# Optimization experiments

Measured on AMD Instinct MI355X. Metric: run time of the kernel, lower is better.

## Reference

```python
import jax, jax.numpy as jnp
import numpy as np

B, S, D, H = 8, 384, 1024, 16
MAX_SEQ_LEN = 512  # XLRelativePositionalEncoding default -> table rows = 2*512-1 = 1023


def setup_inputs() -> dict:
    key = jax.random.key(0)
    ks = jax.random.split(key, 6)
    x = jax.random.normal(ks[0], (B, S, D), jnp.float32)
    qkv_w = jax.random.normal(ks[1], (D, 3 * D), jnp.float32) / np.float32(np.sqrt(D))
    qkv_b = jnp.zeros((3 * D,), jnp.float32)
    out_w = jax.random.normal(ks[2], (D, D), jnp.float32) / np.float32(np.sqrt(D))
    out_b = jnp.zeros((D,), jnp.float32)
    rpe_table = jax.random.normal(ks[3], (2 * MAX_SEQ_LEN - 1, D), jnp.float32) * 0.02
    return {"x": x, "qkv_w": qkv_w, "qkv_b": qkv_b, "out_w": out_w, "out_b": out_b, "rpe_table": rpe_table}


def reference(x, qkv_w, qkv_b, out_w, out_b, rpe_table):
    b, s, d = x.shape
    h = H
    hd = d // h  # head dim (d_k)

    # XL relative positional embeddings: rpe[i, j] = j - i + s, looked up in table
    pe = jnp.arange(s)
    rpe_idx = (pe[None, :] - pe[:, None]) + s  # (s, s) int indices
    rpem = rpe_table[rpe_idx]                   # (s, s, d)
    rpem = rpem.reshape(h, s, s, hd)            # same raw reshape as source

    # QKV projection
    qkv = x @ qkv_w + qkv_b                     # (b, s, 3d)
    qkv = qkv.reshape(b, s, h, 3 * hd).transpose(0, 2, 1, 3)  # (b, h, s, 3*hd)
    q, k, v = jnp.split(qkv, 3, axis=-1)        # each (b, h, s, hd)

    # scaled dot-product with XL relative bias
    scale = jnp.float32(1.0) / jnp.sqrt(jnp.float32(hd))
    logits = jnp.einsum('bhsd,bhkd->bhsk', q, k) * scale
    logits = logits + jnp.einsum('bhsd,hskd->bhsk', q, rpem)
    attention = jax.nn.softmax(logits, axis=-1)  # (b, h, s, s)
    values = jnp.einsum('bhsk,bhkd->bhsd', attention, v)

    values = values.transpose(0, 2, 1, 3).reshape(b, s, d)
    out = values @ out_w + out_b                 # (b, s, d)
    return out, attention
```

## Files before the change

### kernel.cpp

```cpp
#include <hip/hip_runtime.h>

#define S_ 384
#define D_ 1024
#define H_ 16
#define HD_ 64

typedef short bf16x8 __attribute__((ext_vector_type(8)));
typedef float f32x4 __attribute__((ext_vector_type(4)));

#define LDS_AS3(p) ((__attribute__((address_space(3))) unsigned int*)(p))
#define GLB_AS1(p) ((const __attribute__((address_space(1))) unsigned int*)(p))

__device__ __forceinline__ unsigned short f32_to_bf16(float f) {
  unsigned u = __float_as_uint(f);
  u += 0x7FFFu + ((u >> 16) & 1u);
  return (unsigned short)(u >> 16);
}
__device__ __forceinline__ float bf16_to_f32(unsigned short h) {
  return __uint_as_float(((unsigned)h) << 16);
}

__global__ void cast_kernel(const float* __restrict__ src,
                            unsigned short* __restrict__ dst, int n4) {
  int i = blockIdx.x * blockDim.x + threadIdx.x;
  if (i >= n4) return;
  float4 v = ((const float4*)src)[i];
  ushort4 o;
  o.x = f32_to_bf16(v.x); o.y = f32_to_bf16(v.y);
  o.z = f32_to_bf16(v.z); o.w = f32_to_bf16(v.w);
  ((ushort4*)dst)[i] = o;
}

__global__ void transpose_cast_kernel(const float* __restrict__ W,
                                      unsigned short* __restrict__ Wt,
                                      int K, int N) {
  __shared__ float tile[32][33];
  int n0 = blockIdx.x * 32, k0 = blockIdx.y * 32;
  int tx = threadIdx.x, ty = threadIdx.y;
#pragma unroll
  for (int yy = 0; yy < 32; yy += 8)
    tile[ty + yy][tx] = W[(size_t)(k0 + ty + yy) * N + n0 + tx];
  __syncthreads();
#pragma unroll
  for (int yy = 0; yy < 32; yy += 8)
    Wt[(size_t)(n0 + ty + yy) * K + k0 + tx] = f32_to_bf16(tile[tx][ty + yy]);
}

template <int MODE>
__global__ __launch_bounds__(256) void gemm_bt_kernel(
    const unsigned short* __restrict__ A, const unsigned short* __restrict__ Bt,
    const float* __restrict__ bias, unsigned short* __restrict__ Qb,
    unsigned short* __restrict__ Kb, unsigned short* __restrict__ Vt,
    float* __restrict__ Cout) {
  const int K = 1024;
  __shared__ __align__(16) unsigned short As[128 * 32];
  __shared__ __align__(16) unsigned short Bs[128 * 32];
  const int tid = threadIdx.x;
  const int m0 = blockIdx.x * 128, n0 = blockIdx.y * 128;
  const int wid = tid >> 6, lane = tid & 63;
  const int wr = wid >> 1, wc = wid & 1;
  const int l15 = lane & 15, lg = lane >> 4;

  const int r0 = tid >> 2, kk0 = (tid & 3) * 8;
  const int r1 = (256 + tid) >> 2, kk1 = (tid & 3) * 8;

  f32x4 acc[4][4];
#pragma unroll
  for (int m = 0; m < 4; ++m)
#pragma unroll
    for (int n = 0; n < 4; ++n) acc[m][n] = (f32x4){0.f, 0.f, 0.f, 0.f};

  for (int k0 = 0; k0 < K; k0 += 32) {
    __syncthreads();
    {
      char* asb = (char*)As + (wid << 10);
      char* bsb = (char*)Bs + (wid << 10);
      __builtin_amdgcn_global_load_lds(
          GLB_AS1(&A[(size_t)(m0 + r0) * K + k0 + kk0]), LDS_AS3(asb), 16, 0, 0);
      __builtin_amdgcn_global_load_lds(
          GLB_AS1(&Bt[(size_t)(n0 + r0) * K + k0 + kk0]), LDS_AS3(bsb), 16, 0, 0);
      __builtin_amdgcn_global_load_lds(
          GLB_AS1(&A[(size_t)(m0 + r1) * K + k0 + kk1]), LDS_AS3(asb + 4096), 16, 0, 0);
      __builtin_amdgcn_global_load_lds(
          GLB_AS1(&Bt[(size_t)(n0 + r1) * K + k0 + kk1]), LDS_AS3(bsb + 4096), 16, 0, 0);
    }
    __syncthreads();
    bf16x8 af[4], bf[4];
#pragma unroll
    for (int m = 0; m < 4; ++m)
      af[m] = *(bf16x8*)&As[(wr * 64 + m * 16 + l15) * 32 + lg * 8];
#pragma unroll
    for (int n = 0; n < 4; ++n)
      bf[n] = *(bf16x8*)&Bs[(wc * 64 + n * 16 + l15) * 32 + lg * 8];
#pragma unroll
    for (int m = 0; m < 4; ++m)
#pragma unroll
      for (int n = 0; n < 4; ++n)
        acc[m][n] =
            __builtin_amdgcn_mfma_f32_16x16x32_bf16(af[m], bf[n], acc[m][n], 0, 0, 0);
  }

#pragma unroll
  for (int m = 0; m < 4; ++m) {
#pragma unroll
    for (int n = 0; n < 4; ++n) {
#pragma unroll
      for (int r = 0; r < 4; ++r) {
        int R = m0 + wr * 64 + m * 16 + lg * 4 + r;
        int c = n0 + wc * 64 + n * 16 + l15;
        float val = acc[m][n][r] + bias[c];
        if (MODE == 0) {
          int b = R / S_, s = R % S_;
          int hh = c / 192, rr = c % 192;
          int sel = rr >> 6, dd = rr & 63;
          unsigned short bv = f32_to_bf16(val);
          if (sel == 0) {
            Qb[((size_t)(b * H_ + hh) * S_ + s) * HD_ + dd] = bv;
          } else if (sel == 1) {
            Kb[((size_t)(b * H_ + hh) * S_ + s) * HD_ + dd] = bv;
          } else {
            Vt[((size_t)(b * H_ + hh) * HD_ + dd) * S_ + s] = bv;
          }
        } else {
          Cout[(size_t)R * D_ + c] = val;
        }
      }
    }
  }
}

__global__ __launch_bounds__(512) void bias_kernel(
    const unsigned short* __restrict__ Qb, const unsigned short* __restrict__ Tb,
    unsigned short* __restrict__ biasout) {
  __shared__ __align__(16) unsigned short tb[8][8][136];
  const int hh = blockIdx.x;
  const int itile = blockIdx.y;
  const int jz = blockIdx.z;
  const int tid = threadIdx.x;
  const int wid = tid >> 6, lane = tid & 63;
  const int l15 = lane & 15, lg = lane >> 4;
  const int C = 384 - 24 * hh - itile;
  const int i0 = itile * 16;

#pragma unroll
  for (int t = 0; t < 2; ++t) {
    const int il = wid * 2 + t;
    const int i = i0 + il;
    const int b8 = l15 & 7;
    const size_t qaddr = ((size_t)(b8 * H_ + hh) * S_ + i) * HD_ + lg * 8;
    bf16x8 a0 = *(const bf16x8*)&Qb[qaddr];
    bf16x8 a1 = *(const bf16x8*)&Qb[qaddr + 32];
    const int rbase = il * 24 + C;
#pragma unroll
    for (int jrel = 0; jrel < 8; ++jrel) {
      const int jH = jz * 8 + jrel;
      const unsigned short* trow = Tb + (size_t)(rbase + jH) * D_;
      bf16x8 b0 = *(const bf16x8*)&trow[l15 * 64 + lg * 8];
      bf16x8 b1 = *(const bf16x8*)&trow[l15 * 64 + 32 + lg * 8];
      f32x4 d = {0.f, 0.f, 0.f, 0.f};
      d = __builtin_amdgcn_mfma_f32_16x16x32_bf16(a0, b0, d, 0, 0, 0);
      d = __builtin_amdgcn_mfma_f32_16x16x32_bf16(a1, b1, d, 0, 0, 0);
      if (lg < 2) {
#pragma unroll
        for (int rr = 0; rr < 4; ++rr)
          tb[wid][lg * 4 + rr][jrel * 16 + l15] = f32_to_bf16(d[rr]);
      }
    }
    __syncthreads();
    {
      const int b = lane >> 3;
      const int jseg = (lane & 7) * 16;
      uint4 v0 = *(const uint4*)&tb[wid][b][jseg];
      uint4 v1 = *(const uint4*)&tb[wid][b][jseg + 8];
      unsigned short* dst =
          &biasout[(((size_t)(b * H_ + hh)) * S_ + i) * S_ + jz * 128 + jseg];
      *(uint4*)dst = v0;
      *(uint4*)&dst[8] = v1;
    }
    __syncthreads();
  }
}

__global__ __launch_bounds__(256) void attn2_kernel(
    const unsigned short* __restrict__ Qb, const unsigned short* __restrict__ Kb,
    const unsigned short* __restrict__ Vt, const unsigned short* __restrict__ Bias,
    float* __restrict__ attn_out, unsigned short* __restrict__ Vals) {
  __shared__ float lgs[16][392];
  __shared__ __align__(16) unsigned short pb[16][392];
  const int bh = blockIdx.x;
  const int itile = blockIdx.y;
  const int i0 = itile * 16;
  const size_t base = (size_t)bh * (S_ * HD_);
  const int tid = threadIdx.x, wid = tid >> 6, lane = tid & 63;
  const int l15 = lane & 15, lg = lane >> 4;

  {
    const unsigned short* bsrc = Bias + ((size_t)bh * S_ + i0) * S_;
#pragma unroll
    for (int it = 0; it < 3; ++it) {
      int e = it * 256 + tid;
      int row = e / 48, col = (e % 48) * 8;
      *(uint4*)&pb[row][col] = *(const uint4*)&bsrc[(size_t)row * S_ + col];
    }
  }

  const size_t qaddr = base + (size_t)(i0 + l15) * HD_ + lg * 8;
  bf16x8 qa0 = *(const bf16x8*)&Qb[qaddr];
  bf16x8 qa1 = *(const bf16x8*)&Qb[qaddr + 32];
  __syncthreads();

#pragma unroll
  for (int t = 0; t < 6; ++t) {
    const int jH = wid * 6 + t;
    const int j0 = jH * 16;
    const size_t kaddr = base + (size_t)(j0 + l15) * HD_ + lg * 8;
    bf16x8 kb0 = *(const bf16x8*)&Kb[kaddr];
    bf16x8 kb1 = *(const bf16x8*)&Kb[kaddr + 32];
    f32x4 d = {0.f, 0.f, 0.f, 0.f};
    d = __builtin_amdgcn_mfma_f32_16x16x32_bf16(qa0, kb0, d, 0, 0, 0);
    d = __builtin_amdgcn_mfma_f32_16x16x32_bf16(qa1, kb1, d, 0, 0, 0);
#pragma unroll
    for (int rr = 0; rr < 4; ++rr) {
      const int il = lg * 4 + rr;
      lgs[il][j0 + l15] = d[rr] * 0.125f + bf16_to_f32(pb[il][j0 + l15]);
    }
  }
  __syncthreads();

  {
    const int row = tid >> 4, l16 = tid & 15;
    float m = -1e30f;
    for (int j = l16; j < S_; j += 16) m = fmaxf(m, lgs[row][j]);
#pragma unroll
    for (int o = 8; o; o >>= 1) m = fmaxf(m, __shfl_xor(m, o, 16));
    float s = 0.f;
    for (int j = l16; j < S_; j += 16) {
      float e = __expf(lgs[row][j] - m);
      lgs[row][j] = e;
      s += e;
    }
#pragma unroll
    for (int o = 8; o; o >>= 1) s += __shfl_xor(s, o, 16);
    const float inv = 1.0f / s;
    float* ao = attn_out + ((size_t)bh * S_ + i0 + row) * S_;
    for (int j = l16; j < S_; j += 16) {
      float p = lgs[row][j] * inv;
      ao[j] = p;
      pb[row][j] = f32_to_bf16(p);
    }
  }
  __syncthreads();

  {
    const int d0 = wid * 16;
    f32x4 acc = {0.f, 0.f, 0.f, 0.f};
#pragma unroll 4
    for (int kc = 0; kc < 12; ++kc) {
      bf16x8 pa = *(const bf16x8*)&pb[l15][kc * 32 + lg * 8];
      bf16x8 vb = *(const bf16x8*)&Vt[base + (size_t)(d0 + l15) * S_ + kc * 32 + lg * 8];
      acc = __builtin_amdgcn_mfma_f32_16x16x32_bf16(pa, vb, acc, 0, 0, 0);
    }
    const int b = bh >> 4, hh = bh & 15;
#pragma unroll
    for (int rr = 0; rr < 4; ++rr) {
      const int il = lg * 4 + rr;
      Vals[((size_t)(b * S_ + i0 + il)) * D_ + hh * HD_ + d0 + l15] =
          f32_to_bf16(acc[rr]);
    }
  }
}

extern "C" void kernel_launch(void* const* d_in, const int* in_sizes, int n_in,
                              void* d_out, int out_size, void* d_ws,
                              size_t ws_size, hipStream_t stream) {
  (void)in_sizes; (void)n_in; (void)out_size; (void)ws_size;
  const float* x     = (const float*)d_in[0];
  const float* qkv_w = (const float*)d_in[1];
  const float* qkv_b = (const float*)d_in[2];
  const float* out_w = (const float*)d_in[3];
  const float* out_b = (const float*)d_in[4];
  const float* rpe   = (const float*)d_in[5];

  float* out  = (float*)d_out;
  float* attn = out + 3145728;

  unsigned short* ws  = (unsigned short*)d_ws;
  unsigned short* xb  = ws;
  unsigned short* Wt  = xb + 3145728;
  unsigned short* Wot = Wt + 3145728;
  unsigned short* Tb  = Wot + 1048576;
  unsigned short* Qb  = Tb + 1047552;
  unsigned short* Kb  = Qb + 3145728;
  unsigned short* Vt  = Kb + 3145728;
  unsigned short* Vals = Vt + 3145728;
  unsigned short* Bias = Vals + 3145728;

  cast_kernel<<<3072, 256, 0, stream>>>(x, xb, 786432);
  cast_kernel<<<1023, 256, 0, stream>>>(rpe, Tb, 261888);
  transpose_cast_kernel<<<dim3(96, 32), dim3(32, 8), 0, stream>>>(qkv_w, Wt, 1024, 3072);
  transpose_cast_kernel<<<dim3(32, 32), dim3(32, 8), 0, stream>>>(out_w, Wot, 1024, 1024);

  gemm_bt_kernel<0><<<dim3(24, 24), 256, 0, stream>>>(xb, Wt, qkv_b, Qb, Kb, Vt, nullptr);

  bias_kernel<<<dim3(16, 24, 3), 512, 0, stream>>>(Qb, Tb, Bias);

  attn2_kernel<<<dim3(128, 24), 256, 0, stream>>>(Qb, Kb, Vt, Bias, attn, Vals);

  gemm_bt_kernel<1><<<dim3(24, 8), 256, 0, stream>>>(Vals, Wot, out_b, nullptr, nullptr, nullptr, out);
}
```

Measured before the change: 264.6 us.

## Fuse prep cast kernels and double attention row tile to reuse K/V

Merges the two cast and two transpose-cast launches into one prep kernel, removing three launches. The attention kernel now handles 32 query rows per block instead of 16, so each K and V fragment loaded from global memory feeds two MFMA row tiles. The bias is preloaded into the fp32 logits buffer, which is then reused as bf16 storage for the probabilities. This halves the attention grid and raises LDS use per block, which may lower occupancy.

```diff
diff --git a/kernel.cpp b/kernel.cpp
--- a/kernel.cpp
+++ b/kernel.cpp
@@ -20,30 +20,39 @@
   return __uint_as_float(((unsigned)h) << 16);
 }
 
-__global__ void cast_kernel(const float* __restrict__ src,
-                            unsigned short* __restrict__ dst, int n4) {
-  int i = blockIdx.x * blockDim.x + threadIdx.x;
-  if (i >= n4) return;
-  float4 v = ((const float4*)src)[i];
-  ushort4 o;
-  o.x = f32_to_bf16(v.x); o.y = f32_to_bf16(v.y);
-  o.z = f32_to_bf16(v.z); o.w = f32_to_bf16(v.w);
-  ((ushort4*)dst)[i] = o;
-}
-
-__global__ void transpose_cast_kernel(const float* __restrict__ W,
-                                      unsigned short* __restrict__ Wt,
-                                      int K, int N) {
+__global__ __launch_bounds__(256) void prep_kernel(
+    const float* __restrict__ x, const float* __restrict__ rpe,
+    const float* __restrict__ qkv_w, const float* __restrict__ out_w,
+    unsigned short* __restrict__ xb, unsigned short* __restrict__ Tb,
+    unsigned short* __restrict__ Wt, unsigned short* __restrict__ Wot) {
   __shared__ float tile[32][33];
-  int n0 = blockIdx.x * 32, k0 = blockIdx.y * 32;
-  int tx = threadIdx.x, ty = threadIdx.y;
-#pragma unroll
-  for (int yy = 0; yy < 32; yy += 8)
-    tile[ty + yy][tx] = W[(size_t)(k0 + ty + yy) * N + n0 + tx];
-  __syncthreads();
-#pragma unroll
-  for (int yy = 0; yy < 32; yy += 8)
-    Wt[(size_t)(n0 + ty + yy) * K + k0 + tx] = f32_to_bf16(tile[tx][ty + yy]);
+  const int bx = blockIdx.x;
+  const int tid = threadIdx.x;
+  if (bx < 4095) {
+    const float* src = (bx < 3072) ? x : rpe;
+    unsigned short* dst = (bx < 3072) ? xb : Tb;
+    int i = (bx < 3072 ? bx : bx - 3072) * 256 + tid;
+    float4 v = ((const float4*)src)[i];
+    ushort4 o;
+    o.x = f32_to_bf16(v.x); o.y = f32_to_bf16(v.y);
+    o.z = f32_to_bf16(v.z); o.w = f32_to_bf16(v.w);
+    ((ushort4*)dst)[i] = o;
+  } else {
+    const float* W; unsigned short* WT; int N, bb;
+    if (bx < 7167) { W = qkv_w; WT = Wt; N = 3072; bb = bx - 4095; }
+    else           { W = out_w; WT = Wot; N = 1024; bb = bx - 7167; }
+    const int K = 1024;
+    const int nblk = N / 32;
+    const int n0 = (bb % nblk) * 32, k0 = (bb / nblk) * 32;
+    const int tx = tid & 31, ty = tid >> 5;
+#pragma unroll
+    for (int yy = 0; yy < 32; yy += 8)
+      tile[ty + yy][tx] = W[(size_t)(k0 + ty + yy) * N + n0 + tx];
+    __syncthreads();
+#pragma unroll
+    for (int yy = 0; yy < 32; yy += 8)
+      WT[(size_t)(n0 + ty + yy) * K + k0 + tx] = f32_to_bf16(tile[tx][ty + yy]);
+  }
 }
 
 template <int MODE>
@@ -181,54 +190,69 @@
   }
 }
 
-__global__ __launch_bounds__(256) void attn2_kernel(
+__global__ __launch_bounds__(256) void attn3_kernel(
     const unsigned short* __restrict__ Qb, const unsigned short* __restrict__ Kb,
     const unsigned short* __restrict__ Vt, const unsigned short* __restrict__ Bias,
     float* __restrict__ attn_out, unsigned short* __restrict__ Vals) {
-  __shared__ float lgs[16][392];
-  __shared__ __align__(16) unsigned short pb[16][392];
+  __shared__ float lgs[32][408];
   const int bh = blockIdx.x;
-  const int itile = blockIdx.y;
-  const int i0 = itile * 16;
+  const int it32 = blockIdx.y;
+  const int i0 = it32 * 32;
   const size_t base = (size_t)bh * (S_ * HD_);
   const int tid = threadIdx.x, wid = tid >> 6, lane = tid & 63;
   const int l15 = lane & 15, lg = lane >> 4;
 
+  bf16x8 qa[2][2];
+#pragma unroll
+  for (int mt = 0; mt < 2; ++mt) {
+    const size_t qaddr = base + (size_t)(i0 + mt * 16 + l15) * HD_ + lg * 8;
+    qa[mt][0] = *(const bf16x8*)&Qb[qaddr];
+    qa[mt][1] = *(const bf16x8*)&Qb[qaddr + 32];
+  }
+
   {
     const unsigned short* bsrc = Bias + ((size_t)bh * S_ + i0) * S_;
 #pragma unroll
-    for (int it = 0; it < 3; ++it) {
+    for (int it = 0; it < 6; ++it) {
       int e = it * 256 + tid;
-      int row = e / 48, col = (e % 48) * 8;
-      *(uint4*)&pb[row][col] = *(const uint4*)&bsrc[(size_t)row * S_ + col];
-    }
-  }
-
-  const size_t qaddr = base + (size_t)(i0 + l15) * HD_ + lg * 8;
-  bf16x8 qa0 = *(const bf16x8*)&Qb[qaddr];
-  bf16x8 qa1 = *(const bf16x8*)&Qb[qaddr + 32];
+      int row = e / 48, c8 = (e % 48) * 8;
+      ushort4 v0 = *(const ushort4*)&bsrc[(size_t)row * S_ + c8];
+      ushort4 v1 = *(const ushort4*)&bsrc[(size_t)row * S_ + c8 + 4];
+      float4 f0 = {bf16_to_f32(v0.x), bf16_to_f32(v0.y),
+                   bf16_to_f32(v0.z), bf16_to_f32(v0.w)};
+      float4 f1 = {bf16_to_f32(v1.x), bf16_to_f32(v1.y),
+                   bf16_to_f32(v1.z), bf16_to_f32(v1.w)};
+      *(float4*)&lgs[row][c8] = f0;
+      *(float4*)&lgs[row][c8 + 4] = f1;
+    }
+  }
   __syncthreads();
 
 #pragma unroll
   for (int t = 0; t < 6; ++t) {
-    const int jH = wid * 6 + t;
-    const int j0 = jH * 16;
+    const int j0 = (wid * 6 + t) * 16;
     const size_t kaddr = base + (size_t)(j0 + l15) * HD_ + lg * 8;
     bf16x8 kb0 = *(const bf16x8*)&Kb[kaddr];
     bf16x8 kb1 = *(const bf16x8*)&Kb[kaddr + 32];
-    f32x4 d = {0.f, 0.f, 0.f, 0.f};
-    d = __builtin_amdgcn_mfma_f32_16x16x32_bf16(qa0, kb0, d, 0, 0, 0);
-    d = __builtin_amdgcn_mfma_f32_16x16x32_bf16(qa1, kb1, d, 0, 0, 0);
-#pragma unroll
-    for (int rr = 0; rr < 4; ++rr) {
-      const int il = lg * 4 + rr;
-      lgs[il][j0 + l15] = d[rr] * 0.125f + bf16_to_f32(pb[il][j0 + l15]);
+#pragma unroll
+    for (int mt = 0; mt < 2; ++mt) {
+      f32x4 d = {0.f, 0.f, 0.f, 0.f};
+      d = __builtin_amdgcn_mfma_f32_16x16x32_bf16(qa[mt][0], kb0, d, 0, 0, 0);
+      d = __builtin_amdgcn_mfma_f32_16x16x32_bf16(qa[mt][1], kb1, d, 0, 0, 0);
+#pragma unroll
+      for (int rr = 0; rr < 4; ++rr) {
+        const int il = mt * 16 + lg * 4 + rr;
+        lgs[il][j0 + l15] = fmaf(d[rr], 0.125f, lgs[il][j0 + l15]);
+      }
     }
   }
   __syncthreads();
 
-  {
-    const int row = tid >> 4, l16 = tid & 15;
+  unsigned short* us = (unsigned short*)&lgs[0][0];
+#pragma unroll
+  for (int p = 0; p < 2; ++p) {
+    const int row = p * 16 + (tid >> 4);
+    const int l16 = tid & 15;
     float m = -1e30f;
     for (int j = l16; j < S_; j += 16) m = fmaxf(m, lgs[row][j]);
 #pragma unroll
@@ -244,29 +268,36 @@
     const float inv = 1.0f / s;
     float* ao = attn_out + ((size_t)bh * S_ + i0 + row) * S_;
     for (int j = l16; j < S_; j += 16) {
-      float p = lgs[row][j] * inv;
-      ao[j] = p;
-      pb[row][j] = f32_to_bf16(p);
+      float pv = lgs[row][j] * inv;
+      ao[j] = pv;
+      us[row * 816 + j] = f32_to_bf16(pv);
     }
   }
   __syncthreads();
 
   {
     const int d0 = wid * 16;
-    f32x4 acc = {0.f, 0.f, 0.f, 0.f};
-#pragma unroll 4
+    f32x4 acc[2] = {{0.f, 0.f, 0.f, 0.f}, {0.f, 0.f, 0.f, 0.f}};
+#pragma unroll
     for (int kc = 0; kc < 12; ++kc) {
-      bf16x8 pa = *(const bf16x8*)&pb[l15][kc * 32 + lg * 8];
-      bf16x8 vb = *(const bf16x8*)&Vt[base + (size_t)(d0 + l15) * S_ + kc * 32 + lg * 8];
-      acc = __builtin_amdgcn_mfma_f32_16x16x32_bf16(pa, vb, acc, 0, 0, 0);
+      bf16x8 vb =
+          *(const bf16x8*)&Vt[base + (size_t)(d0 + l15) * S_ + kc * 32 + lg * 8];
+#pragma unroll
+      for (int mt = 0; mt < 2; ++mt) {
+        bf16x8 pa =
+            *(const bf16x8*)&us[(size_t)(mt * 16 + l15) * 816 + kc * 32 + lg * 8];
+        acc[mt] = __builtin_amdgcn_mfma_f32_16x16x32_bf16(pa, vb, acc[mt], 0, 0, 0);
+      }
     }
     const int b = bh >> 4, hh = bh & 15;
 #pragma unroll
-    for (int rr = 0; rr < 4; ++rr) {
-      const int il = lg * 4 + rr;
-      Vals[((size_t)(b * S_ + i0 + il)) * D_ + hh * HD_ + d0 + l15] =
-          f32_to_bf16(acc[rr]);
-    }
+    for (int mt = 0; mt < 2; ++mt)
+#pragma unroll
+      for (int rr = 0; rr < 4; ++rr) {
+        const int il = mt * 16 + lg * 4 + rr;
+        Vals[((size_t)(b * S_ + i0 + il)) * D_ + hh * HD_ + d0 + l15] =
+            f32_to_bf16(acc[mt][rr]);
+      }
   }
 }
 
@@ -295,16 +326,13 @@
   unsigned short* Vals = Vt + 3145728;
   unsigned short* Bias = Vals + 3145728;
 
-  cast_kernel<<<3072, 256, 0, stream>>>(x, xb, 786432);
-  cast_kernel<<<1023, 256, 0, stream>>>(rpe, Tb, 261888);
-  transpose_cast_kernel<<<dim3(96, 32), dim3(32, 8), 0, stream>>>(qkv_w, Wt, 1024, 3072);
-  transpose_cast_kernel<<<dim3(32, 32), dim3(32, 8), 0, stream>>>(out_w, Wot, 1024, 1024);
+  prep_kernel<<<8191, 256, 0, stream>>>(x, rpe, qkv_w, out_w, xb, Tb, Wt, Wot);
 
   gemm_bt_kernel<0><<<dim3(24, 24), 256, 0, stream>>>(xb, Wt, qkv_b, Qb, Kb, Vt, nullptr);
 
   bias_kernel<<<dim3(16, 24, 3), 512, 0, stream>>>(Qb, Tb, Bias);
 
-  attn2_kernel<<<dim3(128, 24), 256, 0, stream>>>(Qb, Kb, Vt, Bias, attn, Vals);
+  attn3_kernel<<<dim3(128, 12), 256, 0, stream>>>(Qb, Kb, Vt, Bias, attn, Vals);
 
   gemm_bt_kernel<1><<<dim3(24, 8), 256, 0, stream>>>(Vals, Wot, out_b, nullptr, nullptr, nullptr, out);
 }
```

Result: faster. 256.0 us (-3.2%).
